# Kernel optimization log

Hardware: AMD Instinct MI355X
Metric: run time of the kernel (lower is better)

The kernel has to match this reference:

```python
import jax, jax.numpy as jnp
import numpy as np

INPUT_SIZE = 4
SEQ = 256
EMB = 64
QKV = 64
BATCH = 64
INDICES = np.array([0, 0, 1, 1])
BLK = SEQ // INPUT_SIZE                      # 64 positions per block
POS_GROUP = np.repeat(INDICES, BLK)          # per-position group id, shape [SEQ]
NUM_HEADS = len(np.unique(INDICES))          # 2
GROUP_POS = [np.where(POS_GROUP == g)[0] for g in range(NUM_HEADS)]  # static index sets


def _linear_params(key, din, dout):
    # torch nn.Linear default init: U(-1/sqrt(din), 1/sqrt(din))
    kw, kb = jax.random.split(key)
    s = 1.0 / np.sqrt(din)
    W = jax.random.uniform(kw, (dout, din), jnp.float32, -s, s)
    b = jax.random.uniform(kb, (dout,), jnp.float32, -s, s)
    return W, b


def setup_inputs() -> dict:
    key = jax.random.key(0)
    keys = jax.random.split(key, 1 + 3 * NUM_HEADS)
    inp = {"x": jax.random.normal(keys[0], (BATCH, SEQ, EMB), jnp.float32)}
    for g in range(NUM_HEADS):
        L = len(GROUP_POS[g])                # 128
        din, dout = L * EMB, L * QKV         # 8192 -> 8192
        WQ, bQ = _linear_params(keys[1 + 3 * g + 0], din, dout)
        WK, bK = _linear_params(keys[1 + 3 * g + 1], din, dout)
        WV, bV = _linear_params(keys[1 + 3 * g + 2], din, dout)
        inp[f"WQ{g}"], inp[f"bQ{g}"] = WQ, bQ
        inp[f"WK{g}"], inp[f"bK{g}"] = WK, bK
        inp[f"WV{g}"], inp[f"bV{g}"] = WV, bV
    return inp


def _head(xs, WQ, bQ, WK, bK, WV, bV, L):
    # xs: [B, L*EMB] flattened group slice
    B = xs.shape[0]
    Q = (xs @ WQ.T + bQ).reshape(B, L, QKV)
    K = (xs @ WK.T + bK).reshape(B, L, QKV)
    V = (xs @ WV.T + bV).reshape(B, L, QKV)
    scores = jnp.einsum("bik,bjk->bij", Q, K)        # [B, L, L]
    # Original uses nn.Softmax(dim=1): normalize over the QUERY axis (axis=1).
    attn = jax.nn.softmax(scores, axis=1)
    Z = jnp.einsum("bij,bjk->bik", attn, V)
    # coeff applied AFTER attention @ V, as in the original
    return Z * (1.0 / jnp.sqrt(jnp.float32(QKV)))


def reference(x, WQ0, bQ0, WK0, bK0, WV0, bV0, WQ1, bQ1, WK1, bK1, WV1, bV1):
    params = [(WQ0, bQ0, WK0, bK0, WV0, bV0), (WQ1, bQ1, WK1, bK1, WV1, bV1)]
    B = x.shape[0]
    out = jnp.zeros((B, SEQ, QKV), jnp.float32)
    for g in range(NUM_HEADS):                        # small static loop over groups
        pos = GROUP_POS[g]
        L = len(pos)
        xs = x[:, pos, :].reshape(B, L * EMB)
        Z = _head(xs, *params[g], L)
        out = out.at[:, pos, :].set(Z)
    return out
```

## Files before the change

kernel.cpp:

```cpp
#include <hip/hip_runtime.h>
#include <hip/hip_bf16.h>

#define BATCH 64
#define SEQ   256
#define EMB   64
#define QKVD  64
#define KD    8192
#define ND    8192
#define SEQD  16384
#define BK    64
#define NCHUNK (KD / BK)

typedef __attribute__((ext_vector_type(8))) short bf16x8;
typedef __attribute__((ext_vector_type(4))) float f32x4;

struct WArgs { const float* W[6]; const float* b[6]; };

__device__ __forceinline__ short f2bf(float f) {
    unsigned u = __builtin_bit_cast(unsigned, f);
    u += 0x7fffu + ((u >> 16) & 1u);
    return (short)(u >> 16);
}

__device__ __forceinline__ void gl16(const void* g, void* l) {
    __builtin_amdgcn_global_load_lds(
        (const __attribute__((address_space(1))) void*)g,
        (__attribute__((address_space(3))) void*)l, 16, 0, 0);
}

__device__ __forceinline__ void barrier_fenced() {
    asm volatile("" ::: "memory");
    __builtin_amdgcn_s_barrier();
    asm volatile("" ::: "memory");
}

__global__ __launch_bounds__(256)
void cvt_x_kernel(const float* __restrict__ x, short* __restrict__ xb) {
    const int i = (blockIdx.x * 256 + threadIdx.x) * 4;
    float4 v = *reinterpret_cast<const float4*>(x + i);
    short4 o;
    o.x = f2bf(v.x); o.y = f2bf(v.y); o.z = f2bf(v.z); o.w = f2bf(v.w);
    *reinterpret_cast<short4*>(xb + i) = o;
}

__global__ __launch_bounds__(256, 3)
void qkv_gemm_kernel(const short* __restrict__ xb, WArgs wa,
                     float* __restrict__ qkv) {
    __shared__ __attribute__((aligned(16))) short A_lds[2][64 * 64];
    __shared__ __attribute__((aligned(16))) float W_lds[2][64 * 64];

    const int bid     = blockIdx.x;
    const int logical = (bid & 7) * 96 + (bid >> 3);
    const int gi      = logical >> 7;
    const int n0      = (logical & 127) * 64;
    const int g       = gi / 3;

    const int wv = threadIdx.x >> 6;
    const int ln = threadIdx.x & 63;
    const int r  = ln & 15;
    const int kb = ln >> 4;

    const float* __restrict__ Wg = wa.W[gi];

    const int a_m = ln >> 3;
    const int a_c = (ln & 7) ^ (ln >> 3);
    const int w_r = ln >> 4;

    f32x4 acc0 = {0.f, 0.f, 0.f, 0.f};
    f32x4 acc1 = acc0, acc2 = acc0, acc3 = acc0;

    auto stage = [&](int t, int buf) {
        const short* As = xb + g * KD + t * BK;
        #pragma unroll
        for (int ii = 0; ii < 2; ++ii) {
            const int i = wv * 2 + ii;
            const short* src = As + (size_t)(i * 8 + a_m) * SEQD + a_c * 8;
            gl16(src, (char*)&A_lds[buf][0] + i * 1024);
        }
        const float* Ws = Wg + (size_t)n0 * KD + t * BK;
        #pragma unroll
        for (int jj = 0; jj < 4; ++jj) {
            const int j = wv * 4 + jj;
            const int nrow = j * 4 + w_r;
            const int c = (ln & 15) ^ (nrow & 7);
            const float* src = Ws + (size_t)nrow * KD + c * 4;
            gl16(src, (char*)&W_lds[buf][0] + j * 1024);
        }
    };

    auto compute = [&](int buf) {
        const short* Ab = &A_lds[buf][0];
        const float* Wb = &W_lds[buf][0];
        const int wrow = wv * 16 + r;
        #pragma unroll
        for (int kk = 0; kk < 2; ++kk) {
            const int c0 = kk * 8 + kb * 2;
            f32x4 w0 = *(const f32x4*)(Wb + wrow * 64 + ((c0       ^ (r & 7)) * 4));
            f32x4 w1 = *(const f32x4*)(Wb + wrow * 64 + (((c0 + 1) ^ (r & 7)) * 4));
            bf16x8 bb;
            bb[0] = f2bf(w0[0]); bb[1] = f2bf(w0[1]); bb[2] = f2bf(w0[2]); bb[3] = f2bf(w0[3]);
            bb[4] = f2bf(w1[0]); bb[5] = f2bf(w1[1]); bb[6] = f2bf(w1[2]); bb[7] = f2bf(w1[3]);
            const int ac = ((kk * 4 + kb) ^ (r & 7)) * 8;
            const bf16x8 a0 = *(const bf16x8*)(Ab + (0 * 16 + r) * 64 + ac);
            const bf16x8 a1 = *(const bf16x8*)(Ab + (1 * 16 + r) * 64 + ac);
            const bf16x8 a2 = *(const bf16x8*)(Ab + (2 * 16 + r) * 64 + ac);
            const bf16x8 a3 = *(const bf16x8*)(Ab + (3 * 16 + r) * 64 + ac);
            acc0 = __builtin_amdgcn_mfma_f32_16x16x32_bf16(a0, bb, acc0, 0, 0, 0);
            acc1 = __builtin_amdgcn_mfma_f32_16x16x32_bf16(a1, bb, acc1, 0, 0, 0);
            acc2 = __builtin_amdgcn_mfma_f32_16x16x32_bf16(a2, bb, acc2, 0, 0, 0);
            acc3 = __builtin_amdgcn_mfma_f32_16x16x32_bf16(a3, bb, acc3, 0, 0, 0);
        }
    };

    stage(0, 0);
    stage(1, 1);

    for (int t = 0; t < NCHUNK - 1; ++t) {
        asm volatile("s_waitcnt vmcnt(6)" ::: "memory");
        barrier_fenced();
        compute(t & 1);
        barrier_fenced();
        if (t + 2 < NCHUNK) stage(t + 2, t & 1);
    }
    asm volatile("s_waitcnt vmcnt(0)" ::: "memory");
    barrier_fenced();
    compute((NCHUNK - 1) & 1);

    const int nbr = n0 + wv * 16 + r;
    const float bias = wa.b[gi][nbr];
    float* orow = qkv + (size_t)gi * (BATCH * ND) + nbr;
    #pragma unroll
    for (int reg = 0; reg < 4; ++reg) {
        const int m = kb * 4 + reg;
        orow[(size_t)(m)      * ND] = acc0[reg] + bias;
        orow[(size_t)(m + 16) * ND] = acc1[reg] + bias;
        orow[(size_t)(m + 32) * ND] = acc2[reg] + bias;
        orow[(size_t)(m + 48) * ND] = acc3[reg] + bias;
    }
}

__global__ __launch_bounds__(256)
void attn_kernel(const float* __restrict__ qkv, float* __restrict__ out) {
    __shared__ float Ql[128 * 65];
    __shared__ float Kl[128 * 65];
    __shared__ float Sc[128 * 129];
    __shared__ float Pm[256];
    __shared__ float Ps[256];
    __shared__ float Rden[128];

    const int b = blockIdx.x;
    const int g = blockIdx.y;
    const int t = threadIdx.x;

    const float* __restrict__ Qg = qkv + ((size_t)(3 * g + 0) * BATCH + b) * ND;
    const float* __restrict__ Kg = qkv + ((size_t)(3 * g + 1) * BATCH + b) * ND;
    const float* __restrict__ Vg = qkv + ((size_t)(3 * g + 2) * BATCH + b) * ND;

    for (int e = t; e < 8192; e += 256) {
        const int i = e >> 6, k = e & 63;
        Ql[i * 65 + k] = Qg[e];
        Kl[i * 65 + k] = Kg[e];
    }
    __syncthreads();

    {
        const int i0 = (t >> 4) * 8;
        const int j0 = (t & 15) * 8;
        float s[8][8];
        #pragma unroll
        for (int rr = 0; rr < 8; ++rr)
            #pragma unroll
            for (int cc = 0; cc < 8; ++cc) s[rr][cc] = 0.f;
        for (int k = 0; k < 64; ++k) {
            float qv[8], kv[8];
            #pragma unroll
            for (int rr = 0; rr < 8; ++rr) qv[rr] = Ql[(i0 + rr) * 65 + k];
            #pragma unroll
            for (int cc = 0; cc < 8; ++cc) kv[cc] = Kl[(j0 + cc) * 65 + k];
            #pragma unroll
            for (int rr = 0; rr < 8; ++rr)
                #pragma unroll
                for (int cc = 0; cc < 8; ++cc)
                    s[rr][cc] = fmaf(qv[rr], kv[cc], s[rr][cc]);
        }
        #pragma unroll
        for (int rr = 0; rr < 8; ++rr)
            #pragma unroll
            for (int cc = 0; cc < 8; ++cc)
                Sc[(i0 + rr) * 129 + (j0 + cc)] = s[rr][cc];
    }
    __syncthreads();

    const int j = t & 127, h = t >> 7;
    {
        for (int e = t; e < 8192; e += 256) {
            const int i = e >> 6, k = e & 63;
            Ql[i * 65 + k] = Vg[e];
        }
        float m = -3.0e38f;
        for (int i = h * 64; i < h * 64 + 64; ++i)
            m = fmaxf(m, Sc[i * 129 + j]);
        Pm[h * 128 + j] = m;
    }
    __syncthreads();
    {
        const float m = fmaxf(Pm[j], Pm[128 + j]);
        float sum = 0.f;
        for (int i = h * 64; i < h * 64 + 64; ++i) {
            const float e = __expf(Sc[i * 129 + j] - m);
            Sc[i * 129 + j] = e;
            sum += e;
        }
        Ps[h * 128 + j] = sum;
    }
    __syncthreads();
    if (t < 128) Rden[t] = 1.0f / (Ps[t] + Ps[128 + t]);
    __syncthreads();

    {
        const int i0 = (t >> 4) * 8;
        const int k0 = (t & 15) * 4;
        float z[8][4];
        #pragma unroll
        for (int rr = 0; rr < 8; ++rr)
            #pragma unroll
            for (int cc = 0; cc < 4; ++cc) z[rr][cc] = 0.f;
        for (int jj = 0; jj < 128; ++jj) {
            const float rd = Rden[jj];
            float av[8], vv[4];
            #pragma unroll
            for (int rr = 0; rr < 8; ++rr) av[rr] = Sc[(i0 + rr) * 129 + jj] * rd;
            #pragma unroll
            for (int cc = 0; cc < 4; ++cc) vv[cc] = Ql[jj * 65 + k0 + cc];
            #pragma unroll
            for (int rr = 0; rr < 8; ++rr)
                #pragma unroll
                for (int cc = 0; cc < 4; ++cc)
                    z[rr][cc] = fmaf(av[rr], vv[cc], z[rr][cc]);
        }
        float* op = out + (size_t)b * (SEQ * QKVD) + (size_t)(g * 128) * QKVD + k0;
        #pragma unroll
        for (int rr = 0; rr < 8; ++rr) {
            float4 o;
            o.x = z[rr][0] * 0.125f; o.y = z[rr][1] * 0.125f;
            o.z = z[rr][2] * 0.125f; o.w = z[rr][3] * 0.125f;
            *reinterpret_cast<float4*>(op + (size_t)(i0 + rr) * QKVD) = o;
        }
    }
}

extern "C" void kernel_launch(void* const* d_in, const int* in_sizes, int n_in,
                              void* d_out, int out_size, void* d_ws, size_t ws_size,
                              hipStream_t stream) {
    const float* x = (const float*)d_in[0];
    WArgs wa;
    for (int g = 0; g < 2; ++g)
        for (int q = 0; q < 3; ++q) {
            wa.W[g * 3 + q] = (const float*)d_in[1 + g * 6 + q * 2];
            wa.b[g * 3 + q] = (const float*)d_in[2 + g * 6 + q * 2];
        }

    short* xb  = (short*)d_ws;
    float* qkv = (float*)((char*)d_ws + (size_t)4 * 1024 * 1024);

    cvt_x_kernel<<<dim3(1024), dim3(256), 0, stream>>>(x, xb);
    qkv_gemm_kernel<<<dim3(768), dim3(256), 0, stream>>>(xb, wa, qkv);
    attn_kernel<<<dim3(BATCH, 2), dim3(256), 0, stream>>>(qkv, (float*)d_out);
}
```

Before: 355.9 us.

## Read activations from global directly and stage only weights with wave-local pipelining

The GEMM no longer stages the bf16 activation tile in LDS. Each wave reads A fragments straight from global memory, where they should mostly hit L2. Only the fp32 weight tile is staged, now with a K depth of 128. Because each wave only consumes the weight rows it loaded itself, the loop drops to one barrier per iteration: the next stage is issued before the current compute, and a per-wave vmcnt wait replaces the pre-compute barrier. The trade-off is more scattered global loads for A, lower occupancy (launch bound 3→2) and larger LDS tiles, in exchange for fewer barriers and less LDS traffic.

Result: slower. 515.1 us (median of 2 runs) (+44.7%).

```diff
diff --git a/kernel.cpp b/kernel.cpp
--- a/kernel.cpp
+++ b/kernel.cpp
@@ -8,8 +8,8 @@
 #define KD    8192
 #define ND    8192
 #define SEQD  16384
-#define BK    64
-#define NCHUNK (KD / BK)
+#define BK    128
+#define NT    (KD / BK)
 
 typedef __attribute__((ext_vector_type(8))) short bf16x8;
 typedef __attribute__((ext_vector_type(4))) float f32x4;
@@ -43,11 +43,10 @@
     *reinterpret_cast<short4*>(xb + i) = o;
 }
 
-__global__ __launch_bounds__(256, 3)
+__global__ __launch_bounds__(256, 2)
 void qkv_gemm_kernel(const short* __restrict__ xb, WArgs wa,
                      float* __restrict__ qkv) {
-    __shared__ __attribute__((aligned(16))) short A_lds[2][64 * 64];
-    __shared__ __attribute__((aligned(16))) float W_lds[2][64 * 64];
+    __shared__ __attribute__((aligned(16))) float W_lds[2][64 * BK];
 
     const int bid     = blockIdx.x;
     const int logical = (bid & 7) * 96 + (bid >> 3);
@@ -62,49 +61,43 @@
 
     const float* __restrict__ Wg = wa.W[gi];
 
-    const int a_m = ln >> 3;
-    const int a_c = (ln & 7) ^ (ln >> 3);
-    const int w_r = ln >> 4;
+    const int s_rh = ln >> 5;
+    const int s_c  = ln & 31;
 
     f32x4 acc0 = {0.f, 0.f, 0.f, 0.f};
     f32x4 acc1 = acc0, acc2 = acc0, acc3 = acc0;
 
     auto stage = [&](int t, int buf) {
-        const short* As = xb + g * KD + t * BK;
-        #pragma unroll
-        for (int ii = 0; ii < 2; ++ii) {
-            const int i = wv * 2 + ii;
-            const short* src = As + (size_t)(i * 8 + a_m) * SEQD + a_c * 8;
-            gl16(src, (char*)&A_lds[buf][0] + i * 1024);
-        }
         const float* Ws = Wg + (size_t)n0 * KD + t * BK;
         #pragma unroll
-        for (int jj = 0; jj < 4; ++jj) {
-            const int j = wv * 4 + jj;
-            const int nrow = j * 4 + w_r;
-            const int c = (ln & 15) ^ (nrow & 7);
-            const float* src = Ws + (size_t)nrow * KD + c * 4;
-            gl16(src, (char*)&W_lds[buf][0] + j * 1024);
+        for (int jj = 0; jj < 8; ++jj) {
+            const int j   = wv * 8 + jj;
+            const int row = 2 * j + s_rh;
+            const int c   = s_c ^ (row & 7);
+            gl16(Ws + (size_t)row * KD + c * 4,
+                 (char*)&W_lds[buf][0] + j * 1024);
         }
     };
 
-    auto compute = [&](int buf) {
-        const short* Ab = &A_lds[buf][0];
+    auto compute = [&](int buf, int t) {
         const float* Wb = &W_lds[buf][0];
+        const short* Ag = xb + g * KD + t * BK + kb * 8;
         const int wrow = wv * 16 + r;
-        #pragma unroll
-        for (int kk = 0; kk < 2; ++kk) {
+        const float* Wrow = Wb + wrow * BK;
+        const int sw = (wrow & 7);
+        #pragma unroll
+        for (int kk = 0; kk < 4; ++kk) {
             const int c0 = kk * 8 + kb * 2;
-            f32x4 w0 = *(const f32x4*)(Wb + wrow * 64 + ((c0       ^ (r & 7)) * 4));
-            f32x4 w1 = *(const f32x4*)(Wb + wrow * 64 + (((c0 + 1) ^ (r & 7)) * 4));
+            f32x4 w0 = *(const f32x4*)(Wrow + ((c0    ) ^ sw) * 4);
+            f32x4 w1 = *(const f32x4*)(Wrow + ((c0 + 1) ^ sw) * 4);
             bf16x8 bb;
             bb[0] = f2bf(w0[0]); bb[1] = f2bf(w0[1]); bb[2] = f2bf(w0[2]); bb[3] = f2bf(w0[3]);
             bb[4] = f2bf(w1[0]); bb[5] = f2bf(w1[1]); bb[6] = f2bf(w1[2]); bb[7] = f2bf(w1[3]);
-            const int ac = ((kk * 4 + kb) ^ (r & 7)) * 8;
-            const bf16x8 a0 = *(const bf16x8*)(Ab + (0 * 16 + r) * 64 + ac);
-            const bf16x8 a1 = *(const bf16x8*)(Ab + (1 * 16 + r) * 64 + ac);
-            const bf16x8 a2 = *(const bf16x8*)(Ab + (2 * 16 + r) * 64 + ac);
-            const bf16x8 a3 = *(const bf16x8*)(Ab + (3 * 16 + r) * 64 + ac);
+            const short* ak = Ag + kk * 32;
+            const bf16x8 a0 = *(const bf16x8*)(ak + (size_t)(r)      * SEQD);
+            const bf16x8 a1 = *(const bf16x8*)(ak + (size_t)(r + 16) * SEQD);
+            const bf16x8 a2 = *(const bf16x8*)(ak + (size_t)(r + 32) * SEQD);
+            const bf16x8 a3 = *(const bf16x8*)(ak + (size_t)(r + 48) * SEQD);
             acc0 = __builtin_amdgcn_mfma_f32_16x16x32_bf16(a0, bb, acc0, 0, 0, 0);
             acc1 = __builtin_amdgcn_mfma_f32_16x16x32_bf16(a1, bb, acc1, 0, 0, 0);
             acc2 = __builtin_amdgcn_mfma_f32_16x16x32_bf16(a2, bb, acc2, 0, 0, 0);
@@ -113,18 +106,14 @@
     };
 
     stage(0, 0);
-    stage(1, 1);
-
-    for (int t = 0; t < NCHUNK - 1; ++t) {
-        asm volatile("s_waitcnt vmcnt(6)" ::: "memory");
+    for (int t = 0; t < NT - 1; ++t) {
+        stage(t + 1, (t + 1) & 1);
+        asm volatile("s_waitcnt vmcnt(8)" ::: "memory");
+        compute(t & 1, t);
         barrier_fenced();
-        compute(t & 1);
-        barrier_fenced();
-        if (t + 2 < NCHUNK) stage(t + 2, t & 1);
     }
     asm volatile("s_waitcnt vmcnt(0)" ::: "memory");
-    barrier_fenced();
-    compute((NCHUNK - 1) & 1);
+    compute((NT - 1) & 1, NT - 1);
 
     const int nbr = n0 + wv * 16 + r;
     const float bias = wa.b[gi][nbr];
```
